# Optimization experiments

Hardware: AMD Instinct MI355X
Metric: run time of the kernel (lower is better)

Reference implementation:

```python
import math
import jax, jax.numpy as jnp
import numpy as np

N_HEADS = 16
N_KV_HEADS = 4
HEAD_DIM = 64
DIM = 1024
WINDOW = 16
EPS = 0.01


def _alibi_slopes(n_heads):
    closest = 2 ** math.floor(math.log2(n_heads))
    base = 2.0 ** (-2.0 ** (-(math.log2(closest) - 3)))
    slopes = base ** np.arange(1, closest + 1, dtype=np.float32)
    if closest < n_heads:
        eb = 2.0 ** (-2.0 ** (-(math.log2(2 * closest) - 3)))
        extra = eb ** np.arange(1, 2 * (n_heads - closest) + 1, 2, dtype=np.float32)
        slopes = np.concatenate([slopes, extra])
    return jnp.asarray(slopes[:n_heads])


def _rmsnorm(x, w):
    xf = x.astype(jnp.float32)
    norm = jax.lax.rsqrt(jnp.mean(xf * xf, axis=-1, keepdims=True) + EPS)
    return (xf * norm).astype(x.dtype) * w


def setup_inputs() -> dict:
    key = jax.random.key(0)
    ks = jax.random.split(key, 6)
    B, L = 2, 2048
    s = 1.0 / math.sqrt(DIM)
    return {
        "x": jax.random.normal(ks[0], (B, L, DIM), jnp.float32),
        "wq": jax.random.normal(ks[1], (N_HEADS * HEAD_DIM, DIM), jnp.float32) * s,
        "wk": jax.random.normal(ks[2], (N_KV_HEADS * HEAD_DIM, DIM), jnp.float32) * s,
        "wv": jax.random.normal(ks[3], (N_KV_HEADS * HEAD_DIM, DIM), jnp.float32) * s,
        "wo": jax.random.normal(ks[4], (DIM, N_HEADS * HEAD_DIM), jnp.float32) * s,
        "q_norm_w": jnp.ones((HEAD_DIM,), jnp.float32),
        "k_norm_w": jnp.ones((HEAD_DIM,), jnp.float32),
    }


def reference(x, wq, wk, wv, wo, q_norm_w, k_norm_w):
    B, L, _ = x.shape
    n_rep = N_HEADS // N_KV_HEADS
    q = (x @ wq.T).reshape(B, L, N_HEADS, HEAD_DIM)
    k = (x @ wk.T).reshape(B, L, N_KV_HEADS, HEAD_DIM)
    v = (x @ wv.T).reshape(B, L, N_KV_HEADS, HEAD_DIM)
    q = _rmsnorm(q, q_norm_w)
    k = _rmsnorm(k, k_norm_w)
    # GQA repeat: head h maps to kv head (h % n_kv_heads), matching torch expand order
    k = jnp.broadcast_to(k[:, :, None], (B, L, n_rep, N_KV_HEADS, HEAD_DIM)).reshape(B, L, N_HEADS, HEAD_DIM)
    v = jnp.broadcast_to(v[:, :, None], (B, L, n_rep, N_KV_HEADS, HEAD_DIM)).reshape(B, L, N_HEADS, HEAD_DIM)
    # ALiBi bias with causal + sliding-window mask
    pos = jnp.arange(L)
    rel = pos[None, :] - pos[:, None]  # [L, L], j - i
    slopes = _alibi_slopes(N_HEADS)  # [H]
    bias = slopes[:, None, None] * rel[None].astype(jnp.float32)  # [H, L, L]
    masked = (rel > 0) | (rel < -WINDOW)
    bias = jnp.where(masked[None], -jnp.inf, bias)
    scale = 1.0 / math.sqrt(HEAD_DIM)
    attn = jnp.einsum("bqhd,bkhd->bhqk", q, k) * scale + bias[None]
    attn = jax.nn.softmax(attn, axis=-1)
    out = jnp.einsum("bhqk,bkhd->bqhd", attn, v).reshape(B, L, N_HEADS * HEAD_DIM)
    return out @ wo.T
```

## Files before the change

kernel.cpp:

```cpp
#include <hip/hip_runtime.h>
#include <math.h>

#define DIM 1024
#define NH 16
#define NKV 4
#define HD 64
#define WINDOW 16
#define EPS 0.01f

typedef __bf16 bf16_t;
typedef bf16_t bf16x8 __attribute__((ext_vector_type(8)));
typedef bf16_t bf16x4 __attribute__((ext_vector_type(4)));
typedef float f32x4 __attribute__((ext_vector_type(4)));

__global__ __launch_bounds__(256) void f2bf_all(const float* __restrict__ x,
                                                const float* __restrict__ wq,
                                                const float* __restrict__ wk,
                                                const float* __restrict__ wv,
                                                const float* __restrict__ wo,
                                                bf16_t* __restrict__ xb,
                                                bf16_t* __restrict__ wqkvb,
                                                bf16_t* __restrict__ wob) {
  int i = blockIdx.x * blockDim.x + threadIdx.x;
  const float* src;
  bf16_t* dst;
  int off;
  if (i < 1048576) { src = x; dst = xb; off = i; }
  else if (i < 1310720) { src = wq; dst = wqkvb; off = i - 1048576; }
  else if (i < 1376256) { src = wk; dst = wqkvb + (size_t)1024 * DIM; off = i - 1310720; }
  else if (i < 1441792) { src = wv; dst = wqkvb + (size_t)1280 * DIM; off = i - 1376256; }
  else { src = wo; dst = wob; off = i - 1441792; }
  float4 f = ((const float4*)src)[off];
  bf16x4 o = {(bf16_t)f.x, (bf16_t)f.y, (bf16_t)f.z, (bf16_t)f.w};
  ((bf16x4*)dst)[off] = o;
}


#define GEMM_STAGE(buf, Ag, Bg)                                                 \
  {                                                                             \
    _Pragma("unroll")                                                           \
    for (int it = 0; it < 4; it++) {                                            \
      int c = it * 256 + t;                                                     \
      int r = c >> 3;                                                           \
      int kc = ((c & 7) - r) & 7;                                               \
      __builtin_amdgcn_global_load_lds(                                         \
          (const __attribute__((address_space(1))) void*)((Ag) + (size_t)r * K + kc * 8), \
          (__attribute__((address_space(3))) void*)(As[buf] + c * 8), 16, 0, 0); \
    }                                                                           \
    _Pragma("unroll")                                                           \
    for (int it = 0; it < 2; it++) {                                            \
      int c = it * 256 + t;                                                     \
      int r = c >> 3;                                                           \
      int kc = ((c & 7) - r) & 7;                                               \
      __builtin_amdgcn_global_load_lds(                                         \
          (const __attribute__((address_space(1))) void*)((Bg) + (size_t)r * K + kc * 8), \
          (__attribute__((address_space(3))) void*)(Bs[buf] + c * 8), 16, 0, 0); \
    }                                                                           \
  }

#define GEMM_DBUF_LOOP(Aptr, Bptr)                                              \
  {                                                                             \
    const bf16_t* Abase = Aptr + (size_t)row0 * K;                              \
    const bf16_t* Bbase = Bptr + (size_t)col0 * K;                              \
    GEMM_STAGE(0, Abase, Bbase)                                                 \
    const int nIter = K >> 6;                                                   \
    for (int ki = 0; ki < nIter; ki++) {                                        \
      __syncthreads();                                                          \
      if (ki + 1 < nIter)                                                       \
        GEMM_STAGE((ki + 1) & 1, Abase + (ki + 1) * 64, Bbase + (ki + 1) * 64)  \
      const bf16_t* Ab = As[ki & 1];                                            \
      const bf16_t* Bb = Bs[ki & 1];                                            \
      _Pragma("unroll")                                                         \
      for (int h = 0; h < 2; h++) {                                             \
        bf16x8 af[2], bfr[4];                                                   \
        _Pragma("unroll")                                                       \
        for (int mi = 0; mi < 2; mi++) af[mi] = *(const bf16x8*)(Ab + aoff[h][mi]); \
        _Pragma("unroll")                                                       \
        for (int ni = 0; ni < 4; ni++) bfr[ni] = *(const bf16x8*)(Bb + boff[h][ni]); \
        _Pragma("unroll")                                                       \
        for (int mi = 0; mi < 2; mi++)                                          \
          _Pragma("unroll")                                                     \
          for (int ni = 0; ni < 4; ni++)                                        \
            acc[mi][ni] = __builtin_amdgcn_mfma_f32_16x16x32_bf16(af[mi], bfr[ni], \
                                                                  acc[mi][ni], 0, 0, 0); \
      }                                                                         \
    }                                                                           \
  }

#define GEMM_PROLOGUE()                                                         \
  const int t = threadIdx.x;                                                    \
  const int lane = t & 63;                                                      \
  const int wid = t >> 6;                                                       \
  const int row0 = blockIdx.y * 128;                                            \
  const int col0 = blockIdx.x * 64;                                             \
  const int wm = wid * 32;                                                      \
  const int lquad = lane >> 4;                                                  \
  const int lcol = lane & 15;                                                   \
  int aoff[2][2], boff[2][4];                                                   \
  _Pragma("unroll")                                                             \
  for (int h = 0; h < 2; h++) {                                                 \
    _Pragma("unroll")                                                           \
    for (int mi = 0; mi < 2; mi++) {                                            \
      int r = wm + mi * 16 + lcol;                                              \
      aoff[h][mi] = r * 64 + (((h * 4 + lquad) + r) & 7) * 8;                   \
    }                                                                           \
    _Pragma("unroll")                                                           \
    for (int ni = 0; ni < 4; ni++) {                                            \
      int r = ni * 16 + lcol;                                                   \
      boff[h][ni] = r * 64 + (((h * 4 + lquad) + r) & 7) * 8;                   \
    }                                                                           \
  }                                                                             \
  f32x4 acc[2][4] = {};

__global__ __launch_bounds__(256) void gemm_qkv_rms(const bf16_t* __restrict__ A,
                                                    const bf16_t* __restrict__ B,
                                                    bf16_t* __restrict__ C,
                                                    const float* __restrict__ qw,
                                                    const float* __restrict__ kw,
                                                    int M, int N, int K) {
  __shared__ bf16_t As[2][128 * 64];
  __shared__ bf16_t Bs[2][64 * 64];
  GEMM_PROLOGUE()
  GEMM_DBUF_LOOP(A, B)

  const int hcol = blockIdx.x;
  const bool isv = (hcol >= 20);
  float wreg[4];
  if (!isv) {
    const float* wp = (hcol < 16) ? qw : kw;
#pragma unroll
    for (int ni = 0; ni < 4; ni++) wreg[ni] = wp[ni * 16 + lcol];
  }

#pragma unroll
  for (int mi = 0; mi < 2; mi++) {
#pragma unroll
    for (int r = 0; r < 4; r++) {
      float norm = 1.0f;
      if (!isv) {
        float ss = 0.0f;
#pragma unroll
        for (int ni = 0; ni < 4; ni++) ss += acc[mi][ni][r] * acc[mi][ni][r];
#pragma unroll
        for (int off = 8; off >= 1; off >>= 1) ss += __shfl_xor(ss, off);
        norm = rsqrtf(ss * (1.0f / 64.0f) + EPS);
      }
      size_t base = (size_t)(row0 + wm + mi * 16 + lquad * 4 + r) * N + col0 + lcol;
#pragma unroll
      for (int ni = 0; ni < 4; ni++) {
        float v = acc[mi][ni][r] * norm;
        if (!isv) v *= wreg[ni];
        C[base + ni * 16] = (bf16_t)v;
      }
    }
  }
}

template <typename CT>
__global__ __launch_bounds__(256) void gemm_bf16(const bf16_t* __restrict__ A,
                                                 const bf16_t* __restrict__ B,
                                                 CT* __restrict__ C,
                                                 int M, int N, int K) {
  __shared__ bf16_t As[2][128 * 64];
  __shared__ bf16_t Bs[2][64 * 64];
  GEMM_PROLOGUE()
  GEMM_DBUF_LOOP(A, B)

#pragma unroll
  for (int mi = 0; mi < 2; mi++)
#pragma unroll
    for (int ni = 0; ni < 4; ni++) {
      size_t base = (size_t)(row0 + wm + mi * 16 + lquad * 4) * N + col0 + ni * 16 + lcol;
#pragma unroll
      for (int r = 0; r < 4; r++)
        C[base + (size_t)r * N] = (CT)acc[mi][ni][r];
    }
}

#define LKP 72
#define LVP 40

__global__ __launch_bounds__(256) void attn_mfma(const bf16_t* __restrict__ qkv,
                                                 bf16_t* __restrict__ y) {
  __shared__ bf16_t Ks[4][32][LKP];
  __shared__ bf16_t VTs[4][64][LVP];
  __shared__ bf16_t Ps[4][16][LVP];

  const int t = threadIdx.x;
  const int lane = t & 63;
  const int w = t >> 6;
  const int tile = blockIdx.x >> 2;
  const int hgroup = blockIdx.x & 3;
  const int b = tile >> 7;
  const int i0loc = (tile & 127) << 4;
  const int rowbase = b << 11;
  const int rowg0 = rowbase + i0loc;

#pragma unroll
  for (int it = 0; it < 4; it++) {
    int chunk = t + it * 256;
    int kvh = chunk >> 8;
    int key = (chunk >> 3) & 31;
    int dc = chunk & 7;
    int jloc = i0loc - 16 + key;
    int rg = rowbase + (jloc < 0 ? 0 : jloc);
    bf16x8 val = *(const bf16x8*)(qkv + (size_t)rg * 1536 + 1024 + kvh * 64 + dc * 8);
    *(bf16x8*)(&Ks[kvh][key][dc * 8]) = val;
  }
#pragma unroll
  for (int it = 0; it < 4; it++) {
    int idx = t + it * 256;
    int kvh = idx >> 8;
    int key = (idx >> 3) & 31;
    int dc = idx & 7;
    int jloc = i0loc - 16 + key;
    int rg = rowbase + (jloc < 0 ? 0 : jloc);
    bf16x8 val = *(const bf16x8*)(qkv + (size_t)rg * 1536 + 1280 + kvh * 64 + dc * 8);
    int kslot = ((key >> 3) ^ (dc & 3)) * 8 + (key & 7);
#pragma unroll
    for (int e = 0; e < 8; e++) VTs[kvh][dc * 8 + e][kslot] = val[e];
  }
  __syncthreads();

  const int col = lane & 15;
  const int quad = lane >> 4;
  const int h = hgroup * 4 + w;
  const int kvh = w;
  const float slope = exp2f(-0.5f * (float)(h + 1));

  bf16x8 kf[2][2];
#pragma unroll
  for (int kt = 0; kt < 2; kt++)
#pragma unroll
    for (int kc = 0; kc < 2; kc++)
      kf[kt][kc] = *(const bf16x8*)(&Ks[kvh][kt * 16 + col][kc * 32 + quad * 8]);
  bf16x8 vf[4];
#pragma unroll
  for (int nt = 0; nt < 4; nt++) {
    int dim = nt * 16 + col;
    int kchunk = quad ^ ((dim >> 3) & 3);
    vf[nt] = *(const bf16x8*)(&VTs[kvh][dim][kchunk * 8]);
  }

  const bf16_t* qrow = qkv + (size_t)(rowg0 + col) * 1536 + h * 64;
  bf16x8 qf0 = *(const bf16x8*)(qrow + quad * 8);
  bf16x8 qf1 = *(const bf16x8*)(qrow + 32 + quad * 8);

  f32x4 s0 = {}, s1 = {};
  s0 = __builtin_amdgcn_mfma_f32_16x16x32_bf16(qf0, kf[0][0], s0, 0, 0, 0);
  s0 = __builtin_amdgcn_mfma_f32_16x16x32_bf16(qf1, kf[0][1], s0, 0, 0, 0);
  s1 = __builtin_amdgcn_mfma_f32_16x16x32_bf16(qf0, kf[1][0], s1, 0, 0, 0);
  s1 = __builtin_amdgcn_mfma_f32_16x16x32_bf16(qf1, kf[1][1], s1, 0, 0, 0);

  const bool t0dead = (i0loc == 0);
  float sc0[4], sc1[4];
#pragma unroll
  for (int r = 0; r < 4; r++) {
    int rel0 = col - 16 - (quad * 4 + r);
    int rel1 = rel0 + 16;
    bool m0 = t0dead || (rel0 < -WINDOW);
    bool m1 = (rel1 > 0);
    sc0[r] = m0 ? -INFINITY : s0[r] * 0.125f + slope * (float)rel0;
    sc1[r] = m1 ? -INFINITY : s1[r] * 0.125f + slope * (float)rel1;
  }
  float mx[4], sum[4], p0[4], p1[4];
#pragma unroll
  for (int r = 0; r < 4; r++) mx[r] = fmaxf(sc0[r], sc1[r]);
#pragma unroll
  for (int off = 8; off >= 1; off >>= 1)
#pragma unroll
    for (int r = 0; r < 4; r++) mx[r] = fmaxf(mx[r], __shfl_xor(mx[r], off));
#pragma unroll
  for (int r = 0; r < 4; r++) {
    p0[r] = __expf(sc0[r] - mx[r]);
    p1[r] = __expf(sc1[r] - mx[r]);
    sum[r] = p0[r] + p1[r];
  }
#pragma unroll
  for (int off = 8; off >= 1; off >>= 1)
#pragma unroll
    for (int r = 0; r < 4; r++) sum[r] += __shfl_xor(sum[r], off);

#pragma unroll
  for (int r = 0; r < 4; r++) {
    Ps[w][quad * 4 + r][col] = (bf16_t)p0[r];
    Ps[w][quad * 4 + r][16 + col] = (bf16_t)p1[r];
  }
  __syncthreads();
  bf16x8 pf = *(const bf16x8*)(&Ps[w][col][quad * 8]);

  f32x4 o[4] = {};
#pragma unroll
  for (int nt = 0; nt < 4; nt++)
    o[nt] = __builtin_amdgcn_mfma_f32_16x16x32_bf16(pf, vf[nt], o[nt], 0, 0, 0);

#pragma unroll
  for (int nt = 0; nt < 4; nt++)
#pragma unroll
    for (int r = 0; r < 4; r++)
      y[(size_t)(rowg0 + quad * 4 + r) * 1024 + h * 64 + nt * 16 + col] =
          (bf16_t)(o[nt][r] / sum[r]);
}

extern "C" void kernel_launch(void* const* d_in, const int* in_sizes, int n_in,
                              void* d_out, int out_size, void* d_ws, size_t ws_size,
                              hipStream_t stream) {
  const float* x  = (const float*)d_in[0];
  const float* wq = (const float*)d_in[1];
  const float* wk = (const float*)d_in[2];
  const float* wv = (const float*)d_in[3];
  const float* wo = (const float*)d_in[4];
  const float* qw = (const float*)d_in[5];
  const float* kw = (const float*)d_in[6];
  float* out = (float*)d_out;

  const int M = 4096;

  bf16_t* xb    = (bf16_t*)d_ws;
  bf16_t* wqkvb = xb + (size_t)M * DIM;
  bf16_t* wob   = wqkvb + (size_t)1536 * DIM;
  bf16_t* qkv   = wob + (size_t)DIM * DIM;
  bf16_t* yb    = qkv + (size_t)M * 1536;

  dim3 blk(256);
  f2bf_all<<<1703936 / 256, blk, 0, stream>>>(x, wq, wk, wv, wo, xb, wqkvb, wob);

  gemm_qkv_rms<<<dim3(1536 / 64, M / 128), blk, 0, stream>>>(xb, wqkvb, qkv, qw, kw, M, 1536, DIM);

  attn_mfma<<<1024, blk, 0, stream>>>(qkv, yb);

  gemm_bf16<float><<<dim3(DIM / 64, M / 128), blk, 0, stream>>>(yb, wob, out, M, DIM, DIM);
}
```

Before: 131.4 us.

## Process all 16 heads per attention block to share K/V tile loads

The attention kernel now launches 256 blocks of 1024 threads, one wave per head, instead of 1024 blocks that each covered 4 heads. Each block loads the shared 32-key K/V window for all 4 KV heads once, rather than four times across blocks. The barrier between writing and reading each wave's private probability tile is also removed, since only that wave touches it. The change relies on LDS accesses within a single wavefront being ordered. Larger blocks may reduce scheduling flexibility, and this kernel is a small part of the total time.

```diff
diff --git a/kernel.cpp b/kernel.cpp
--- a/kernel.cpp
+++ b/kernel.cpp
@@ -180,52 +180,40 @@
 #define LKP 72
 #define LVP 40
 
-__global__ __launch_bounds__(256) void attn_mfma(const bf16_t* __restrict__ qkv,
-                                                 bf16_t* __restrict__ y) {
+__global__ __launch_bounds__(1024) void attn_mfma(const bf16_t* __restrict__ qkv,
+                                                  bf16_t* __restrict__ y) {
   __shared__ bf16_t Ks[4][32][LKP];
   __shared__ bf16_t VTs[4][64][LVP];
-  __shared__ bf16_t Ps[4][16][LVP];
+  __shared__ bf16_t Ps[16][16][LVP];
 
   const int t = threadIdx.x;
   const int lane = t & 63;
   const int w = t >> 6;
-  const int tile = blockIdx.x >> 2;
-  const int hgroup = blockIdx.x & 3;
-  const int b = tile >> 7;
-  const int i0loc = (tile & 127) << 4;
+  const int b = blockIdx.x >> 7;
+  const int i0loc = (blockIdx.x & 127) << 4;
   const int rowbase = b << 11;
   const int rowg0 = rowbase + i0loc;
 
-#pragma unroll
-  for (int it = 0; it < 4; it++) {
-    int chunk = t + it * 256;
-    int kvh = chunk >> 8;
-    int key = (chunk >> 3) & 31;
-    int dc = chunk & 7;
+  {
+    int kvh = t >> 8;
+    int key = (t >> 3) & 31;
+    int dc = t & 7;
     int jloc = i0loc - 16 + key;
     int rg = rowbase + (jloc < 0 ? 0 : jloc);
-    bf16x8 val = *(const bf16x8*)(qkv + (size_t)rg * 1536 + 1024 + kvh * 64 + dc * 8);
-    *(bf16x8*)(&Ks[kvh][key][dc * 8]) = val;
-  }
-#pragma unroll
-  for (int it = 0; it < 4; it++) {
-    int idx = t + it * 256;
-    int kvh = idx >> 8;
-    int key = (idx >> 3) & 31;
-    int dc = idx & 7;
-    int jloc = i0loc - 16 + key;
-    int rg = rowbase + (jloc < 0 ? 0 : jloc);
-    bf16x8 val = *(const bf16x8*)(qkv + (size_t)rg * 1536 + 1280 + kvh * 64 + dc * 8);
+    const bf16_t* src = qkv + (size_t)rg * 1536 + 1024 + kvh * 64 + dc * 8;
+    bf16x8 kval = *(const bf16x8*)src;
+    *(bf16x8*)(&Ks[kvh][key][dc * 8]) = kval;
+    bf16x8 vval = *(const bf16x8*)(src + 256);
     int kslot = ((key >> 3) ^ (dc & 3)) * 8 + (key & 7);
 #pragma unroll
-    for (int e = 0; e < 8; e++) VTs[kvh][dc * 8 + e][kslot] = val[e];
+    for (int e = 0; e < 8; e++) VTs[kvh][dc * 8 + e][kslot] = vval[e];
   }
   __syncthreads();
 
   const int col = lane & 15;
   const int quad = lane >> 4;
-  const int h = hgroup * 4 + w;
-  const int kvh = w;
+  const int h = w;
+  const int kvh = w & 3;
   const float slope = exp2f(-0.5f * (float)(h + 1));
 
   bf16x8 kf[2][2];
@@ -286,7 +274,6 @@
     Ps[w][quad * 4 + r][col] = (bf16_t)p0[r];
     Ps[w][quad * 4 + r][16 + col] = (bf16_t)p1[r];
   }
-  __syncthreads();
   bf16x8 pf = *(const bf16x8*)(&Ps[w][col][quad * 8]);
 
   f32x4 o[4] = {};
@@ -327,7 +314,7 @@
 
   gemm_qkv_rms<<<dim3(1536 / 64, M / 128), blk, 0, stream>>>(xb, wqkvb, qkv, qw, kw, M, 1536, DIM);
 
-  attn_mfma<<<1024, blk, 0, stream>>>(qkv, yb);
+  attn_mfma<<<256, dim3(1024), 0, stream>>>(qkv, yb);
 
   gemm_bf16<float><<<dim3(DIM / 64, M / 128), blk, 0, stream>>>(yb, wob, out, M, DIM, DIM);
 }
```

Result: faster. 127.9 us (-2.7%).
